# Kernel optimization log

Hardware: AMD Instinct MI355X
Metric: run time of the kernel (lower is better)

Reference implementation:

```python
import jax, jax.numpy as jnp
import numpy as np

D_MODEL = 1024
TEMPERATURE = 1.0

def setup_inputs() -> dict:
    key = jax.random.key(0)
    ks = jax.random.split(key, 9)
    B, NQ, NK, D = 4, 2048, 2048, D_MODEL
    s = 1.0 / np.sqrt(D)
    return {
        "Q": jax.random.normal(ks[0], (B, NQ, D), jnp.float32),
        "K": jax.random.normal(ks[1], (B, NK, D), jnp.float32),
        "V": jax.random.normal(ks[2], (B, NK, D), jnp.float32),
        "Wq": jax.random.normal(ks[3], (D, D), jnp.float32) * s,
        "bq": jax.random.normal(ks[4], (D,), jnp.float32) * 0.01,
        "Wk": jax.random.normal(ks[5], (D, D), jnp.float32) * s,
        "bk": jax.random.normal(ks[6], (D,), jnp.float32) * 0.01,
        "Wv": jax.random.normal(ks[7], (D, D), jnp.float32) * s,
        "bv": jax.random.normal(ks[8], (D,), jnp.float32) * 0.01,
    }

def reference(Q, K, V, Wq, bq, Wk, bk, Wv, bv):
    # torch nn.Linear: y = x @ W.T + b
    Qp = Q @ Wq.T + bq  # [B, NQ, D]
    Kp = K @ Wk.T + bk  # [B, NK, D]
    Vp = V @ Wv.T + bv  # [B, NK, D]

    # use_kl=True branch, vectorized:
    # kl[b,i,j] = D_KL(softmax(Kp[b,j]) || softmax(Qp[b,i]))
    #           = sum_d pK*(log pK - log pQ) = -H(pK_j) - pK_j . log pQ_i
    logpQ = jax.nn.log_softmax(Qp, axis=-1)  # [B, NQ, D]
    logpK = jax.nn.log_softmax(Kp, axis=-1)  # [B, NK, D]
    pK = jnp.exp(logpK)
    neg_ent_K = jnp.sum(pK * logpK, axis=-1)            # [B, NK], = -H(pK)
    cross = jnp.einsum('bjd,bid->bij', pK, logpQ)       # [B, NQ, NK]
    kl = neg_ent_K[:, None, :] - cross                  # [B, NQ, NK]
    scores = -kl / TEMPERATURE

    attn = jax.nn.softmax(scores, axis=-1)              # [B, NQ, NK]
    out = jnp.einsum('bij,bjd->bid', attn, Vp)          # [B, NQ, D]
    return out, attn
```

## Files before the change

### kernel.cpp

```cpp
#include <hip/hip_runtime.h>
#include <math.h>

#define D_MODEL 1024
#define NQS 2048
#define NKS 2048
#define BATCH 4

typedef __attribute__((ext_vector_type(8))) short bf16x8;
typedef __attribute__((ext_vector_type(4))) float f32x4;

#define AS1 __attribute__((address_space(1)))
#define AS3 __attribute__((address_space(3)))

__device__ __forceinline__ unsigned short f2bf(float f) {
  unsigned u = __builtin_bit_cast(unsigned, f);
  u = (u + 0x7FFF + ((u >> 16) & 1)) >> 16;
  return (unsigned short)u;
}
__device__ __forceinline__ float bf2f(unsigned short s) {
  return __builtin_bit_cast(float, ((unsigned)s) << 16);
}

__global__ __launch_bounds__(256) void cvt3_k(
    const float* __restrict__ s0, const float* __restrict__ s1,
    const float* __restrict__ s2, short* __restrict__ d0,
    short* __restrict__ d1, short* __restrict__ d2, int n8)
{
  const int z = blockIdx.z;
  const float* src = z == 0 ? s0 : (z == 1 ? s1 : s2);
  short* dst = z == 0 ? d0 : (z == 1 ? d1 : d2);
  int i = blockIdx.x * 256 + threadIdx.x;
  if (i >= n8) return;
  const float4 a = *(const float4*)&src[(long)i * 8];
  const float4 b = *(const float4*)&src[(long)i * 8 + 4];
  bf16x8 o;
  o[0] = (short)f2bf(a.x); o[1] = (short)f2bf(a.y);
  o[2] = (short)f2bf(a.z); o[3] = (short)f2bf(a.w);
  o[4] = (short)f2bf(b.x); o[5] = (short)f2bf(b.y);
  o[6] = (short)f2bf(b.z); o[7] = (short)f2bf(b.w);
  *(bf16x8*)&dst[(long)i * 8] = o;
}

__device__ __forceinline__ void gemm_tile_body(
    const short* __restrict__ Ab, const short* __restrict__ Bb,
    const float* __restrict__ bias, float bscale, float* __restrict__ Cf,
    short* __restrict__ Cbf, int N, int K, int gm, int gn)
{
  __shared__ short As[2][128 * 32];
  __shared__ short Bs[2][128 * 32];
  const int t = threadIdx.x;
  const int lane = t & 63, w = t >> 6;
  const int wm = w >> 1, wn = w & 1;

  const int srow = lane >> 2, sq = lane & 3;
  const short* gA0 = Ab + (long)(gm + w * 32 + srow) * K + sq * 8;
  const short* gA1 = Ab + (long)(gm + w * 32 + 16 + srow) * K + sq * 8;
  const short* gB0 = Bb + (long)(gn + w * 32 + srow) * K + sq * 8;
  const short* gB1 = Bb + (long)(gn + w * 32 + 16 + srow) * K + sq * 8;
  const int seg0 = (w * 2 + 0) * 512, seg1 = (w * 2 + 1) * 512;

  const int frow = lane & 15, fq = lane >> 4;

  f32x4 acc[4][4] = {};

  for (int k0 = 0; k0 < K; k0 += 64) {
#pragma unroll
    for (int p = 0; p < 2; ++p) {
      const int ko = k0 + p * 32;
      __builtin_amdgcn_global_load_lds((const AS1 void*)(gA0 + ko),
                                       (AS3 void*)(&As[p][seg0]), 16, 0, 0);
      __builtin_amdgcn_global_load_lds((const AS1 void*)(gA1 + ko),
                                       (AS3 void*)(&As[p][seg1]), 16, 0, 0);
      __builtin_amdgcn_global_load_lds((const AS1 void*)(gB0 + ko),
                                       (AS3 void*)(&Bs[p][seg0]), 16, 0, 0);
      __builtin_amdgcn_global_load_lds((const AS1 void*)(gB1 + ko),
                                       (AS3 void*)(&Bs[p][seg1]), 16, 0, 0);
    }
    __syncthreads();
#pragma unroll
    for (int p = 0; p < 2; ++p) {
      bf16x8 af[4], bfm[4];
#pragma unroll
      for (int mi = 0; mi < 4; ++mi)
        af[mi] =
            *(const bf16x8*)&As[p][(wm * 64 + mi * 16 + frow) * 32 + fq * 8];
#pragma unroll
      for (int ni = 0; ni < 4; ++ni)
        bfm[ni] =
            *(const bf16x8*)&Bs[p][(wn * 64 + ni * 16 + frow) * 32 + fq * 8];
#pragma unroll
      for (int mi = 0; mi < 4; ++mi)
#pragma unroll
        for (int ni = 0; ni < 4; ++ni)
          acc[mi][ni] = __builtin_amdgcn_mfma_f32_16x16x32_bf16(
              af[mi], bfm[ni], acc[mi][ni], 0, 0, 0);
    }
    __syncthreads();
  }

  float bb[4];
#pragma unroll
  for (int ni = 0; ni < 4; ++ni)
    bb[ni] = bias ? bias[gn + wn * 64 + ni * 16 + frow] * bscale : 0.f;

#pragma unroll
  for (int mi = 0; mi < 4; ++mi) {
#pragma unroll
    for (int r = 0; r < 4; ++r) {
      const long row = gm + wm * 64 + mi * 16 + fq * 4 + r;
#pragma unroll
      for (int ni = 0; ni < 4; ++ni) {
        const long col = gn + wn * 64 + ni * 16 + frow;
        float v = acc[mi][ni][r] + bb[ni];
        if (Cf) Cf[row * (long)N + col] = v;
        else    Cbf[row * (long)N + col] = (short)f2bf(v);
      }
    }
  }
}

__global__ __launch_bounds__(256, 4) void mfma_abt_k(
    const short* __restrict__ A, const short* __restrict__ B,
    const float* __restrict__ bias, float bscale, float* __restrict__ Cf,
    short* __restrict__ Cbf, int N, int K, long sA, long sB, long sC,
    long sBias, int swap)
{
  const int bz = blockIdx.z;
  const int gm = (swap ? blockIdx.x : blockIdx.y) * 128;
  const int gn = (swap ? blockIdx.y : blockIdx.x) * 128;
  gemm_tile_body(A + (long)bz * sA, B + (long)bz * sB,
                 bias ? bias + (long)bz * sBias : nullptr, bscale,
                 Cf ? Cf + (long)bz * sC : nullptr,
                 Cbf ? Cbf + (long)bz * sC : nullptr, N, K, gm, gn);
}


#define STAGE_HALF(gbase, hoff, kofs, region)                                \
  do {                                                                       \
    __builtin_amdgcn_global_load_lds(                                        \
        (const AS1 void*)((gbase) + (long)(hoff) * K + (kofs)),              \
        (AS3 void*)((region) + w * 512), 16, 0, 0);                          \
    __builtin_amdgcn_global_load_lds(                                        \
        (const AS1 void*)((gbase) + (long)((hoff) + 64) * K + (kofs)),       \
        (AS3 void*)((region) + 4096 + w * 512), 16, 0, 0);                   \
  } while (0)

#define PHASE_TOP()                 \
  __builtin_amdgcn_s_barrier();     \
  __builtin_amdgcn_s_setprio(1)

#define PHASE_END()                 \
  __builtin_amdgcn_s_setprio(0);    \
  __builtin_amdgcn_s_barrier()

template <int PI>
__device__ __forceinline__ void tile4(short (&As)[2][2][8192],
                                      short (&Bs)[2][2][8192],
                                      const short* gA, const short* gB,
                                      f32x4 (&acc)[8][4], int tau, int K,
                                      int w, int wm, int wn, int frow,
                                      int fq, int fr7)
{
  const int kt2 = (tau + 2) << 6;
  const short* Ah = &As[PI][wm][0];
  const short* Bh = &Bs[PI][wn >> 1][0];
  const int bofs = (wn & 1) * 64;
  const int x0 = (fq ^ fr7) * 8;
  const int x1 = ((4 + fq) ^ fr7) * 8;

  bf16x8 a0[4][2], a1[4][2], b0[2][2], b1[2][2];

#pragma unroll
  for (int mi = 0; mi < 4; ++mi) {
    a0[mi][0] = *(const bf16x8*)&Ah[(mi * 16 + frow) * 64 + x0];
    a0[mi][1] = *(const bf16x8*)&Ah[(mi * 16 + frow) * 64 + x1];
  }
#pragma unroll
  for (int ni = 0; ni < 2; ++ni) {
    b0[ni][0] = *(const bf16x8*)&Bh[(bofs + ni * 16 + frow) * 64 + x0];
    b0[ni][1] = *(const bf16x8*)&Bh[(bofs + ni * 16 + frow) * 64 + x1];
  }
  PHASE_TOP();
#pragma unroll
  for (int kk = 0; kk < 2; ++kk)
#pragma unroll
    for (int mi = 0; mi < 4; ++mi)
#pragma unroll
      for (int ni = 0; ni < 2; ++ni)
        acc[mi][ni] = __builtin_amdgcn_mfma_f32_16x16x32_bf16(
            a0[mi][kk], b0[ni][kk], acc[mi][ni], 0, 0, 0);
  PHASE_END();

#pragma unroll
  for (int ni = 0; ni < 2; ++ni) {
    b1[ni][0] = *(const bf16x8*)&Bh[(bofs + 32 + ni * 16 + frow) * 64 + x0];
    b1[ni][1] = *(const bf16x8*)&Bh[(bofs + 32 + ni * 16 + frow) * 64 + x1];
  }
  PHASE_TOP();
#pragma unroll
  for (int kk = 0; kk < 2; ++kk)
#pragma unroll
    for (int mi = 0; mi < 4; ++mi)
#pragma unroll
      for (int ni = 0; ni < 2; ++ni)
        acc[mi][2 + ni] = __builtin_amdgcn_mfma_f32_16x16x32_bf16(
            a0[mi][kk], b1[ni][kk], acc[mi][2 + ni], 0, 0, 0);
  PHASE_END();

#pragma unroll
  for (int mi = 0; mi < 4; ++mi) {
    a1[mi][0] = *(const bf16x8*)&Ah[(64 + mi * 16 + frow) * 64 + x0];
    a1[mi][1] = *(const bf16x8*)&Ah[(64 + mi * 16 + frow) * 64 + x1];
  }
  if (kt2 < K) {
    STAGE_HALF(gB, 0,   kt2, &Bs[PI][0][0]);
    STAGE_HALF(gB, 128, kt2, &Bs[PI][1][0]);
  }
  PHASE_TOP();
#pragma unroll
  for (int kk = 0; kk < 2; ++kk)
#pragma unroll
    for (int mi = 0; mi < 4; ++mi)
#pragma unroll
      for (int ni = 0; ni < 2; ++ni)
        acc[4 + mi][2 + ni] = __builtin_amdgcn_mfma_f32_16x16x32_bf16(
            a1[mi][kk], b1[ni][kk], acc[4 + mi][2 + ni], 0, 0, 0);
  PHASE_END();

  if (kt2 < K) {
    STAGE_HALF(gA, 0,   kt2, &As[PI][0][0]);
    STAGE_HALF(gA, 128, kt2, &As[PI][1][0]);
  }
  __builtin_amdgcn_s_barrier();
  __builtin_amdgcn_s_setprio(1);
#pragma unroll
  for (int kk = 0; kk < 2; ++kk)
#pragma unroll
    for (int mi = 0; mi < 4; ++mi)
#pragma unroll
      for (int ni = 0; ni < 2; ++ni)
        acc[4 + mi][ni] = __builtin_amdgcn_mfma_f32_16x16x32_bf16(
            a1[mi][kk], b0[ni][kk], acc[4 + mi][ni], 0, 0, 0);
  __builtin_amdgcn_s_setprio(0);
  if (kt2 < K) asm volatile("s_waitcnt vmcnt(8)" ::: "memory");
  else         asm volatile("s_waitcnt vmcnt(0)" ::: "memory");
  __builtin_amdgcn_s_barrier();
}

__device__ __forceinline__ void gemm256_body(
    const short* __restrict__ A, const short* __restrict__ B,
    const float* __restrict__ bias, float bscale, float* __restrict__ Cf,
    short* __restrict__ Cbf, int N, int K, int gm, int gn)
{
  __shared__ short As[2][2][8192];
  __shared__ short Bs[2][2][8192];
  const int t = threadIdx.x;
  const int w = t >> 6, l = t & 63;
  const int wm = w >> 2, wn = w & 3;
  const int frow = l & 15, fq = l >> 4, fr7 = l & 7;
  const int srow0 = w * 8 + (l >> 3);
  const int sslot = (l & 7) ^ (l >> 3);

  const short* gA = A + (long)(gm + srow0) * K + sslot * 8;
  const short* gB = B + (long)(gn + srow0) * K + sslot * 8;

  f32x4 acc[8][4] = {};

  STAGE_HALF(gA, 0,   0,  &As[0][0][0]);
  STAGE_HALF(gA, 128, 0,  &As[0][1][0]);
  STAGE_HALF(gB, 0,   0,  &Bs[0][0][0]);
  STAGE_HALF(gB, 128, 0,  &Bs[0][1][0]);
  STAGE_HALF(gA, 0,   64, &As[1][0][0]);
  STAGE_HALF(gA, 128, 64, &As[1][1][0]);
  STAGE_HALF(gB, 0,   64, &Bs[1][0][0]);
  STAGE_HALF(gB, 128, 64, &Bs[1][1][0]);
  asm volatile("s_waitcnt vmcnt(8)" ::: "memory");
  __builtin_amdgcn_s_barrier();

  const int NT = K >> 6;
  for (int tau = 0; tau < NT; tau += 2) {
    tile4<0>(As, Bs, gA, gB, acc, tau, K, w, wm, wn, frow, fq, fr7);
    tile4<1>(As, Bs, gA, gB, acc, tau + 1, K, w, wm, wn, frow, fq, fr7);
  }

  float bb[4];
#pragma unroll
  for (int Ni = 0; Ni < 4; ++Ni)
    bb[Ni] = bias ? bias[gn + wn * 64 + Ni * 16 + frow] * bscale : 0.f;

#pragma unroll
  for (int Mi = 0; Mi < 8; ++Mi) {
#pragma unroll
    for (int r = 0; r < 4; ++r) {
      const long row = gm + wm * 128 + Mi * 16 + fq * 4 + r;
#pragma unroll
      for (int Ni = 0; Ni < 4; ++Ni) {
        const long col = gn + wn * 64 + Ni * 16 + frow;
        float v = acc[Mi][Ni][r] + bb[Ni];
        if (Cf) Cf[row * (long)N + col] = v;
        else    Cbf[row * (long)N + col] = (short)f2bf(v);
      }
    }
  }
}

__global__ __launch_bounds__(512, 2) void mfma8_abt_k(
    const short* __restrict__ A, const short* __restrict__ B,
    const float* __restrict__ bias, float bscale, float* __restrict__ Cf,
    short* __restrict__ Cbf, int N, int K, long sA, long sB, long sC,
    long sBias, int swap)
{
  const int bz = blockIdx.z;
  const int gm = (swap ? blockIdx.x : blockIdx.y) * 256;
  const int gn = (swap ? blockIdx.y : blockIdx.x) * 256;
  gemm256_body(A + (long)bz * sA, B + (long)bz * sB,
               bias ? bias + (long)bz * sBias : nullptr, bscale,
               Cf ? Cf + (long)bz * sC : nullptr,
               Cbf ? Cbf + (long)bz * sC : nullptr, N, K, gm, gn);
}

__global__ __launch_bounds__(512, 2) void mfma8_proj_k(
    const short* __restrict__ Xq, const short* __restrict__ Xk,
    const short* __restrict__ Xv, const short* __restrict__ Wq,
    const short* __restrict__ Wk, const short* __restrict__ Wv,
    const float* __restrict__ bq, const float* __restrict__ bk,
    const float* __restrict__ bv, short* __restrict__ Oq,
    short* __restrict__ Ok, short* __restrict__ Ov)
{
  const int z = blockIdx.z;
  const short* X = z == 0 ? Xq : (z == 1 ? Xk : Xv);
  const short* W = z == 0 ? Wq : (z == 1 ? Wk : Wv);
  const float* bias = z == 0 ? bq : (z == 1 ? bk : bv);
  short* O = z == 0 ? Oq : (z == 1 ? Ok : Ov);
  gemm256_body(X, W, bias, 1.0f, nullptr, O, D_MODEL, D_MODEL,
               blockIdx.x * 256, blockIdx.y * 256);
}

__global__ __launch_bounds__(256) void kstats_k(short* __restrict__ KP,
                                                float* __restrict__ negent)
{
  __shared__ float red[4];
  const long row = blockIdx.x;
  short* x = KP + row * (long)D_MODEL;
  const int t = threadIdx.x;
  short4 raw = *(const short4*)&x[t * 4];
  float v0 = bf2f((unsigned short)raw.x), v1 = bf2f((unsigned short)raw.y);
  float v2 = bf2f((unsigned short)raw.z), v3 = bf2f((unsigned short)raw.w);
  float m = fmaxf(fmaxf(v0, v1), fmaxf(v2, v3));
  for (int o = 32; o; o >>= 1) m = fmaxf(m, __shfl_xor(m, o));
  if ((t & 63) == 0) red[t >> 6] = m;
  __syncthreads();
  m = fmaxf(fmaxf(red[0], red[1]), fmaxf(red[2], red[3]));
  __syncthreads();
  float e0 = __expf(v0 - m), e1 = __expf(v1 - m), e2 = __expf(v2 - m),
        e3 = __expf(v3 - m);
  float s = e0 + e1 + e2 + e3;
  for (int o = 32; o; o >>= 1) s += __shfl_xor(s, o);
  if ((t & 63) == 0) red[t >> 6] = s;
  __syncthreads();
  s = red[0] + red[1] + red[2] + red[3];
  __syncthreads();
  const float inv = 1.0f / s;
  const float lse = m + __logf(s);
  float p0 = e0 * inv, p1 = e1 * inv, p2 = e2 * inv, p3 = e3 * inv;
  float ne = p0 * (v0 - lse) + p1 * (v1 - lse) + p2 * (v2 - lse) +
             p3 * (v3 - lse);
  for (int o = 32; o; o >>= 1) ne += __shfl_xor(ne, o);
  if ((t & 63) == 0) red[t >> 6] = ne;
  __syncthreads();
  if (t == 0) negent[row] = red[0] + red[1] + red[2] + red[3];
  short4 pw;
  pw.x = (short)f2bf(p0); pw.y = (short)f2bf(p1);
  pw.z = (short)f2bf(p2); pw.w = (short)f2bf(p3);
  *(short4*)&x[t * 4] = pw;
}

__global__ __launch_bounds__(256) void asoftmax_k(float* __restrict__ S,
                                                  short* __restrict__ Sbf)
{
  __shared__ float red[4];
  const long row = blockIdx.x;
  float* x = S + row * (long)NKS;
  short* y = Sbf + row * (long)NKS;
  const int t = threadIdx.x;
  float4 v0 = *(const float4*)&x[t * 4];
  float4 v1 = *(const float4*)&x[1024 + t * 4];
  float m = fmaxf(fmaxf(fmaxf(v0.x, v0.y), fmaxf(v0.z, v0.w)),
                  fmaxf(fmaxf(v1.x, v1.y), fmaxf(v1.z, v1.w)));
  for (int o = 32; o; o >>= 1) m = fmaxf(m, __shfl_xor(m, o));
  if ((t & 63) == 0) red[t >> 6] = m;
  __syncthreads();
  m = fmaxf(fmaxf(red[0], red[1]), fmaxf(red[2], red[3]));
  __syncthreads();
  float4 e0 = {__expf(v0.x - m), __expf(v0.y - m), __expf(v0.z - m),
               __expf(v0.w - m)};
  float4 e1 = {__expf(v1.x - m), __expf(v1.y - m), __expf(v1.z - m),
               __expf(v1.w - m)};
  float s = e0.x + e0.y + e0.z + e0.w + e1.x + e1.y + e1.z + e1.w;
  for (int o = 32; o; o >>= 1) s += __shfl_xor(s, o);
  if ((t & 63) == 0) red[t >> 6] = s;
  __syncthreads();
  s = red[0] + red[1] + red[2] + red[3];
  const float inv = 1.0f / s;
  float4 p0 = {e0.x * inv, e0.y * inv, e0.z * inv, e0.w * inv};
  float4 p1 = {e1.x * inv, e1.y * inv, e1.z * inv, e1.w * inv};
  *(float4*)&x[t * 4] = p0;
  *(float4*)&x[1024 + t * 4] = p1;
  short4 b0, b1;
  b0.x = (short)f2bf(p0.x); b0.y = (short)f2bf(p0.y);
  b0.z = (short)f2bf(p0.z); b0.w = (short)f2bf(p0.w);
  b1.x = (short)f2bf(p1.x); b1.y = (short)f2bf(p1.y);
  b1.z = (short)f2bf(p1.z); b1.w = (short)f2bf(p1.w);
  *(short4*)&y[t * 4] = b0;
  *(short4*)&y[1024 + t * 4] = b1;
}

__global__ __launch_bounds__(256) void transpose_k(const short* __restrict__ src,
                                                   short* __restrict__ dst)
{
  __shared__ short tile[64][68];
  const int j0 = blockIdx.x * 64;
  const int d0 = blockIdx.y * 64;
  const int t = threadIdx.x;
  const int r = t >> 2, c = t & 3;
#pragma unroll
  for (int i = 0; i < 4; ++i)
    *(short4*)&tile[r][c * 16 + i * 4] =
        *(const short4*)&src[(long)(j0 + r) * D_MODEL + d0 + c * 16 + i * 4];
  __syncthreads();
  const long b = j0 >> 11;
  const int jj = j0 & 2047;
#pragma unroll
  for (int i = 0; i < 4; ++i) {
    short4 o;
    o.x = tile[c * 16 + i * 4 + 0][r];
    o.y = tile[c * 16 + i * 4 + 1][r];
    o.z = tile[c * 16 + i * 4 + 2][r];
    o.w = tile[c * 16 + i * 4 + 3][r];
    *(short4*)&dst[b * ((long)D_MODEL * NKS) + (long)(d0 + r) * NKS + jj +
                   c * 16 + i * 4] = o;
  }
}

extern "C" void kernel_launch(void* const* d_in, const int* in_sizes, int n_in,
                              void* d_out, int out_size, void* d_ws,
                              size_t ws_size, hipStream_t stream)
{
  const float* Q = (const float*)d_in[0];
  const float* K = (const float*)d_in[1];
  const float* V = (const float*)d_in[2];
  const float* Wq = (const float*)d_in[3];
  const float* bq = (const float*)d_in[4];
  const float* Wk = (const float*)d_in[5];
  const float* bk = (const float*)d_in[6];
  const float* Wv = (const float*)d_in[7];
  const float* bv = (const float*)d_in[8];

  float* out = (float*)d_out;
  float* attn = out + (long)BATCH * NQS * D_MODEL;

  const long SZ = (long)BATCH * NQS * D_MODEL;
  short* ws = (short*)d_ws;
  short* Qbf = ws;
  short* Kbf = ws + SZ;
  short* Vbf = ws + 2 * SZ;
  short* Qp  = ws + 3 * SZ;
  short* pK  = ws + 4 * SZ;
  short* Vp  = ws + 5 * SZ;
  float* negent = (float*)(ws + 6 * SZ);
  short* attn_bf = ws;
  short* Vpt = ws + 2 * SZ;

  short* Wqb = (short*)attn;
  short* Wkb = Wqb + (long)D_MODEL * D_MODEL;
  short* Wvb = Wkb + (long)D_MODEL * D_MODEL;

  dim3 blk(256), blk8(512);
  const int n8x = (int)(SZ / 8);
  const int n8w = D_MODEL * D_MODEL / 8;

  cvt3_k<<<dim3(n8x / 256, 1, 3), blk, 0, stream>>>(Q, K, V, Qbf, Kbf, Vbf,
                                                    n8x);
  cvt3_k<<<dim3(n8w / 256, 1, 3), blk, 0, stream>>>(Wq, Wk, Wv, Wqb, Wkb, Wvb,
                                                    n8w);

  dim3 gp((BATCH * NQS) / 256, D_MODEL / 256, 3);
  mfma8_proj_k<<<gp, blk8, 0, stream>>>(Qbf, Kbf, Vbf, Wqb, Wkb, Wvb, bq, bk,
                                        bv, Qp, pK, Vp);

  kstats_k<<<dim3(BATCH * NKS), blk, 0, stream>>>(pK, negent);

  transpose_k<<<dim3((BATCH * NKS) / 64, D_MODEL / 64), blk, 0, stream>>>(Vp,
                                                                          Vpt);

  dim3 gs(NKS / 256, NQS / 256, BATCH);
  mfma8_abt_k<<<gs, blk8, 0, stream>>>(
      Qp, pK, negent, -1.0f, attn, nullptr, NKS, D_MODEL,
      (long)NQS * D_MODEL, (long)NKS * D_MODEL, (long)NQS * NKS, NKS, 0);

  asoftmax_k<<<dim3(BATCH * NQS), blk, 0, stream>>>(attn, attn_bf);

  dim3 go(NQS / 128, D_MODEL / 128, BATCH);
  mfma_abt_k<<<go, blk, 0, stream>>>(
      attn_bf, Vpt, nullptr, 0.f, out, nullptr, D_MODEL, NKS,
      (long)NQS * NKS, (long)D_MODEL * NKS, (long)NQS * D_MODEL, 0, 1);
}
```

Baseline: 381.6 us.

## Prefetch next k-tile LDS fragments into registers across GEMM tile boundary

Restructures the MFMA main loop so A and B fragments for the next k-tile are read from LDS into persistent registers while the current tile finishes, with B fragment buffers ping-ponged between the two tile phases. Global-to-LDS staging for both operands is issued together after a full vmcnt drain. The aim is to hide LDS read latency behind MFMA work. In exchange it raises VGPR pressure and waits for all outstanding global loads each tile, which may reduce overlap of global traffic.

Measured after the change: 411.1 us. 7.7% more time.

```diff
diff --git a/kernel.cpp b/kernel.cpp
--- a/kernel.cpp
+++ b/kernel.cpp
@@ -145,105 +145,79 @@
         (AS3 void*)((region) + 4096 + w * 512), 16, 0, 0);                   \
   } while (0)
 
-#define PHASE_TOP()                 \
-  __builtin_amdgcn_s_barrier();     \
-  __builtin_amdgcn_s_setprio(1)
-
-#define PHASE_END()                 \
-  __builtin_amdgcn_s_setprio(0);    \
-  __builtin_amdgcn_s_barrier()
+#define MFMA_Q(AF, BF, MO, NO)                                        \
+  do {                                                                \
+    __builtin_amdgcn_s_setprio(1);                                    \
+    _Pragma("unroll") for (int kk = 0; kk < 2; ++kk)                  \
+        _Pragma("unroll") for (int mi = 0; mi < 4; ++mi)              \
+            _Pragma("unroll") for (int ni = 0; ni < 2; ++ni)          \
+                acc[(MO) + mi][(NO) + ni] =                           \
+                    __builtin_amdgcn_mfma_f32_16x16x32_bf16(          \
+                        AF[mi][kk], BF[ni][kk], acc[(MO) + mi][(NO) + ni], \
+                        0, 0, 0);                                     \
+    __builtin_amdgcn_s_setprio(0);                                    \
+  } while (0)
 
 template <int PI>
 __device__ __forceinline__ void tile4(short (&As)[2][2][8192],
                                       short (&Bs)[2][2][8192],
                                       const short* gA, const short* gB,
-                                      f32x4 (&acc)[8][4], int tau, int K,
-                                      int w, int wm, int wn, int frow,
-                                      int fq, int fr7)
-{
-  const int kt2 = (tau + 2) << 6;
-  const short* Ah = &As[PI][wm][0];
-  const short* Bh = &Bs[PI][wn >> 1][0];
+                                      f32x4 (&acc)[8][4],
+                                      bf16x8 (&aA)[4][2], bf16x8 (&aB)[4][2],
+                                      bf16x8 (&b0r)[2][2], bf16x8 (&b1r)[2][2],
+                                      int tau, int NT, int K, int w, int wm,
+                                      int wn, int frow, int fq, int fr7)
+{
+  bf16x8 (&b_cur)[2][2] = PI ? b1r : b0r;
+  bf16x8 (&b_alt)[2][2] = PI ? b0r : b1r;
+  const short* Ah  = &As[PI][wm][0];
+  const short* Bh  = &Bs[PI][wn >> 1][0];
+  const short* Ahn = &As[1 - PI][wm][0];
+  const short* Bhn = &Bs[1 - PI][wn >> 1][0];
   const int bofs = (wn & 1) * 64;
   const int x0 = (fq ^ fr7) * 8;
   const int x1 = ((4 + fq) ^ fr7) * 8;
 
-  bf16x8 a0[4][2], a1[4][2], b0[2][2], b1[2][2];
-
 #pragma unroll
   for (int mi = 0; mi < 4; ++mi) {
-    a0[mi][0] = *(const bf16x8*)&Ah[(mi * 16 + frow) * 64 + x0];
-    a0[mi][1] = *(const bf16x8*)&Ah[(mi * 16 + frow) * 64 + x1];
+    aB[mi][0] = *(const bf16x8*)&Ah[(64 + mi * 16 + frow) * 64 + x0];
+    aB[mi][1] = *(const bf16x8*)&Ah[(64 + mi * 16 + frow) * 64 + x1];
   }
 #pragma unroll
   for (int ni = 0; ni < 2; ++ni) {
-    b0[ni][0] = *(const bf16x8*)&Bh[(bofs + ni * 16 + frow) * 64 + x0];
-    b0[ni][1] = *(const bf16x8*)&Bh[(bofs + ni * 16 + frow) * 64 + x1];
-  }
-  PHASE_TOP();
-#pragma unroll
-  for (int kk = 0; kk < 2; ++kk)
-#pragma unroll
-    for (int mi = 0; mi < 4; ++mi)
-#pragma unroll
-      for (int ni = 0; ni < 2; ++ni)
-        acc[mi][ni] = __builtin_amdgcn_mfma_f32_16x16x32_bf16(
-            a0[mi][kk], b0[ni][kk], acc[mi][ni], 0, 0, 0);
-  PHASE_END();
-
-#pragma unroll
-  for (int ni = 0; ni < 2; ++ni) {
-    b1[ni][0] = *(const bf16x8*)&Bh[(bofs + 32 + ni * 16 + frow) * 64 + x0];
-    b1[ni][1] = *(const bf16x8*)&Bh[(bofs + 32 + ni * 16 + frow) * 64 + x1];
-  }
-  PHASE_TOP();
-#pragma unroll
-  for (int kk = 0; kk < 2; ++kk)
-#pragma unroll
-    for (int mi = 0; mi < 4; ++mi)
-#pragma unroll
-      for (int ni = 0; ni < 2; ++ni)
-        acc[mi][2 + ni] = __builtin_amdgcn_mfma_f32_16x16x32_bf16(
-            a0[mi][kk], b1[ni][kk], acc[mi][2 + ni], 0, 0, 0);
-  PHASE_END();
-
-#pragma unroll
-  for (int mi = 0; mi < 4; ++mi) {
-    a1[mi][0] = *(const bf16x8*)&Ah[(64 + mi * 16 + frow) * 64 + x0];
-    a1[mi][1] = *(const bf16x8*)&Ah[(64 + mi * 16 + frow) * 64 + x1];
-  }
-  if (kt2 < K) {
+    b_alt[ni][0] = *(const bf16x8*)&Bh[(bofs + 32 + ni * 16 + frow) * 64 + x0];
+    b_alt[ni][1] = *(const bf16x8*)&Bh[(bofs + 32 + ni * 16 + frow) * 64 + x1];
+  }
+  __builtin_amdgcn_s_barrier();
+  MFMA_Q(aA, b_cur, 0, 0);
+  __builtin_amdgcn_s_barrier();
+  MFMA_Q(aA, b_alt, 0, 2);
+  __builtin_amdgcn_s_barrier();
+  MFMA_Q(aB, b_alt, 4, 2);
+  __builtin_amdgcn_s_barrier();
+
+  asm volatile("s_waitcnt vmcnt(0)" ::: "memory");
+  if (tau + 1 < NT) {
+#pragma unroll
+    for (int mi = 0; mi < 4; ++mi) {
+      aA[mi][0] = *(const bf16x8*)&Ahn[(mi * 16 + frow) * 64 + x0];
+      aA[mi][1] = *(const bf16x8*)&Ahn[(mi * 16 + frow) * 64 + x1];
+    }
+#pragma unroll
+    for (int ni = 0; ni < 2; ++ni) {
+      b_alt[ni][0] = *(const bf16x8*)&Bhn[(bofs + ni * 16 + frow) * 64 + x0];
+      b_alt[ni][1] = *(const bf16x8*)&Bhn[(bofs + ni * 16 + frow) * 64 + x1];
+    }
+  }
+  if (tau + 2 < NT) {
+    const int kt2 = (tau + 2) << 6;
+    STAGE_HALF(gA, 0,   kt2, &As[PI][0][0]);
+    STAGE_HALF(gA, 128, kt2, &As[PI][1][0]);
     STAGE_HALF(gB, 0,   kt2, &Bs[PI][0][0]);
     STAGE_HALF(gB, 128, kt2, &Bs[PI][1][0]);
   }
-  PHASE_TOP();
-#pragma unroll
-  for (int kk = 0; kk < 2; ++kk)
-#pragma unroll
-    for (int mi = 0; mi < 4; ++mi)
-#pragma unroll
-      for (int ni = 0; ni < 2; ++ni)
-        acc[4 + mi][2 + ni] = __builtin_amdgcn_mfma_f32_16x16x32_bf16(
-            a1[mi][kk], b1[ni][kk], acc[4 + mi][2 + ni], 0, 0, 0);
-  PHASE_END();
-
-  if (kt2 < K) {
-    STAGE_HALF(gA, 0,   kt2, &As[PI][0][0]);
-    STAGE_HALF(gA, 128, kt2, &As[PI][1][0]);
-  }
-  __builtin_amdgcn_s_barrier();
-  __builtin_amdgcn_s_setprio(1);
-#pragma unroll
-  for (int kk = 0; kk < 2; ++kk)
-#pragma unroll
-    for (int mi = 0; mi < 4; ++mi)
-#pragma unroll
-      for (int ni = 0; ni < 2; ++ni)
-        acc[4 + mi][ni] = __builtin_amdgcn_mfma_f32_16x16x32_bf16(
-            a1[mi][kk], b0[ni][kk], acc[4 + mi][ni], 0, 0, 0);
-  __builtin_amdgcn_s_setprio(0);
-  if (kt2 < K) asm volatile("s_waitcnt vmcnt(8)" ::: "memory");
-  else         asm volatile("s_waitcnt vmcnt(0)" ::: "memory");
+  __builtin_amdgcn_s_barrier();
+  MFMA_Q(aB, b_cur, 4, 0);
   __builtin_amdgcn_s_barrier();
 }
 
@@ -264,7 +238,11 @@
   const short* gA = A + (long)(gm + srow0) * K + sslot * 8;
   const short* gB = B + (long)(gn + srow0) * K + sslot * 8;
 
+  const int bofs = (wn & 1) * 64;
+  const int x0 = (fq ^ fr7) * 8, x1 = ((4 + fq) ^ fr7) * 8;
+
   f32x4 acc[8][4] = {};
+  bf16x8 aA[4][2], aB[4][2], b0r[2][2], b1r[2][2];
 
   STAGE_HALF(gA, 0,   0,  &As[0][0][0]);
   STAGE_HALF(gA, 128, 0,  &As[0][1][0]);
@@ -277,10 +255,25 @@
   asm volatile("s_waitcnt vmcnt(8)" ::: "memory");
   __builtin_amdgcn_s_barrier();
 
+#pragma unroll
+  for (int mi = 0; mi < 4; ++mi) {
+    aA[mi][0] = *(const bf16x8*)&As[0][wm][(mi * 16 + frow) * 64 + x0];
+    aA[mi][1] = *(const bf16x8*)&As[0][wm][(mi * 16 + frow) * 64 + x1];
+  }
+#pragma unroll
+  for (int ni = 0; ni < 2; ++ni) {
+    b0r[ni][0] =
+        *(const bf16x8*)&Bs[0][wn >> 1][(bofs + ni * 16 + frow) * 64 + x0];
+    b0r[ni][1] =
+        *(const bf16x8*)&Bs[0][wn >> 1][(bofs + ni * 16 + frow) * 64 + x1];
+  }
+
   const int NT = K >> 6;
   for (int tau = 0; tau < NT; tau += 2) {
-    tile4<0>(As, Bs, gA, gB, acc, tau, K, w, wm, wn, frow, fq, fr7);
-    tile4<1>(As, Bs, gA, gB, acc, tau + 1, K, w, wm, wn, frow, fq, fr7);
+    tile4<0>(As, Bs, gA, gB, acc, aA, aB, b0r, b1r, tau, NT, K, w, wm, wn,
+             frow, fq, fr7);
+    tile4<1>(As, Bs, gA, gB, acc, aA, aB, b0r, b1r, tau + 1, NT, K, w, wm,
+             wn, frow, fq, fr7);
   }
 
   float bb[4];
```
